# Optimization experiments

Measured on AMD Instinct MI355X. Metric: run time of the kernel, lower is better.

Reference implementation:

```python
import jax, jax.numpy as jnp
import numpy as np
import math

HEAD = 4
B, N, C = 8, 1024, 256


def setup_inputs() -> dict:
    key = jax.random.key(0)
    k1, k2, k3, k4, k5 = jax.random.split(key, 5)
    query = jax.random.normal(k1, (B, N, C), dtype=jnp.float32)
    keyt = jax.random.normal(k2, (B, N, C), dtype=jnp.float32)
    value = jax.random.normal(k3, (B, N, C), dtype=jnp.float32)
    mask = jax.random.randint(k4, (B, N, N), 0, 2).astype(bool)
    dis = jax.random.normal(k5, (B, N, N), dtype=jnp.float32)
    return {"query": query, "key": keyt, "value": value, "mask": mask, "dis": dis}


def reference(query, key, value, mask, dis):
    Bq, Nq, Cq = key.shape
    d = Cq // HEAD
    # split heads: [B,N,C] -> [h,B,N,d]
    q = query.reshape(Bq, Nq, HEAD, d).transpose(2, 0, 1, 3)
    k = key.reshape(Bq, Nq, HEAD, d).transpose(2, 0, 1, 3)
    v = value.reshape(Bq, Nq, HEAD, d).transpose(2, 0, 1, 3)
    # scores: [h,B,N,N]; note: dis added BEFORE scaling, as in the torch code
    scores = jnp.einsum('hbnd,hbmd->hbnm', q, k)
    scores = scores + dis[None]            # dis broadcasts over head dim
    scores = scores / math.sqrt(d)
    scores = jnp.where(mask[None], -jnp.inf, scores)
    p_attn = jax.nn.softmax(scores, axis=-1)
    out = jnp.einsum('hbnm,hbmd->hbnd', p_attn, v)  # [h,B,N,d]
    out = out.transpose(1, 2, 0, 3).reshape(Bq, Nq, Cq)
    return out, p_attn
```

## Files before the change

kernel.cpp:

```cpp
#include <hip/hip_runtime.h>
#include <math.h>

#define HEADS 4
#define BATCH 8
#define SEQ   1024
#define CH    256
#define DH    64
#define RB    16
#define NTHR  512
#define SSTR  1032

typedef float  floatx4  __attribute__((ext_vector_type(4)));
typedef short  shortx8  __attribute__((ext_vector_type(8)));

__device__ __forceinline__ unsigned short f2bf(float f) {
    unsigned u = __float_as_uint(f);
    unsigned r = u + 0x7FFFu + ((u >> 16) & 1u);
    return (unsigned short)(r >> 16);
}
__device__ __forceinline__ float bf2f(unsigned short h) {
    return __uint_as_float(((unsigned)h) << 16);
}
__device__ __forceinline__ shortx8 pack8(float4 a, float4 b) {
    shortx8 r;
    r[0] = (short)f2bf(a.x); r[1] = (short)f2bf(a.y);
    r[2] = (short)f2bf(a.z); r[3] = (short)f2bf(a.w);
    r[4] = (short)f2bf(b.x); r[5] = (short)f2bf(b.y);
    r[6] = (short)f2bf(b.z); r[7] = (short)f2bf(b.w);
    return r;
}

__global__ __launch_bounds__(NTHR, 8)
void attn_mfma(const float* __restrict__ q, const float* __restrict__ k,
               const float* __restrict__ v, const void* __restrict__ maskp,
               const float* __restrict__ dis, float* __restrict__ out,
               float* __restrict__ pout)
{
    __shared__ unsigned short Sraw[RB][SSTR];
    __shared__ float Opart[RB][65];
    __shared__ float invs[RB];

    const int t   = threadIdx.x;
    const int bid = blockIdx.x;
    const int nb  = bid & 63;
    const int hb  = bid >> 6;
    const int b   = hb & (BATCH - 1);
    const int h   = hb >> 3;
    const int n0  = nb * RB;

    const int lane = t & 63;
    const int w    = t >> 6;
    const int ln   = lane & 15;
    const int qd   = lane >> 4;

    int fl;
    {
        const unsigned* mw = (const unsigned*)maskp;
        int found = 0;
        #pragma unroll
        for (int j = 0; j < 16; ++j)
            if (mw[lane * 16 + j] & 0xFFFFFF00u) found = 1;
        fl = (__ballot(found != 0) != 0ULL) ? 1 : 0;
    }
    const unsigned char* mask8  = (const unsigned char*)maskp;
    const int*           mask32 = (const int*)maskp;

    const float* qrow = q + ((size_t)(b * SEQ + n0 + ln)) * CH + h * DH;
    shortx8 aq0, aq1;
    {
        float4 a0 = *(const float4*)(qrow + qd * 8);
        float4 a1 = *(const float4*)(qrow + qd * 8 + 4);
        float4 a2 = *(const float4*)(qrow + 32 + qd * 8);
        float4 a3 = *(const float4*)(qrow + 32 + qd * 8 + 4);
        aq0 = pack8(a0, a1);
        aq1 = pack8(a2, a3);
    }

    const float* kbase = k + ((size_t)(b * SEQ)) * CH + h * DH;
    const float* vbase = v + ((size_t)(b * SEQ)) * CH + h * DH;

    #pragma unroll 2
    for (int mc = 0; mc < 8; ++mc) {
        const int mg = mc * 128 + w * 16 + ln;
        const size_t dibase = ((size_t)(b * SEQ + n0 + qd * 4)) * SEQ + mg;
        float dv[4]; int mk[4];
        #pragma unroll
        for (int r = 0; r < 4; ++r) dv[r] = dis[dibase + (size_t)r * SEQ];
        if (fl) {
            #pragma unroll
            for (int r = 0; r < 4; ++r) mk[r] = mask8[dibase + (size_t)r * SEQ];
        } else {
            #pragma unroll
            for (int r = 0; r < 4; ++r) mk[r] = mask32[dibase + (size_t)r * SEQ];
        }
        const float* krow = kbase + (size_t)mg * CH;
        float4 k0 = *(const float4*)(krow + qd * 8);
        float4 k1 = *(const float4*)(krow + qd * 8 + 4);
        float4 k2 = *(const float4*)(krow + 32 + qd * 8);
        float4 k3 = *(const float4*)(krow + 32 + qd * 8 + 4);

        shortx8 b0 = pack8(k0, k1), b1 = pack8(k2, k3);
        floatx4 acc = {0.f, 0.f, 0.f, 0.f};
        acc = __builtin_amdgcn_mfma_f32_16x16x32_bf16(aq0, b0, acc, 0, 0, 0);
        acc = __builtin_amdgcn_mfma_f32_16x16x32_bf16(aq1, b1, acc, 0, 0, 0);
        #pragma unroll
        for (int r = 0; r < 4; ++r) {
            float sc = mk[r] ? -INFINITY : (acc[r] + dv[r]) * 0.125f;
            Sraw[qd * 4 + r][mg] = f2bf(sc);
        }
    }
    __syncthreads();

    {
        const int r = t >> 5, l = t & 31;
        float mx = -INFINITY;
        #pragma unroll
        for (int j = 0; j < 4; ++j) {
            shortx8 sv = *(const shortx8*)&Sraw[r][j * 256 + l * 8];
            #pragma unroll
            for (int e = 0; e < 8; ++e) mx = fmaxf(mx, bf2f((unsigned short)sv[e]));
        }
        #pragma unroll
        for (int off = 16; off; off >>= 1) mx = fmaxf(mx, __shfl_xor(mx, off, 32));
        float sum = 0.f;
        #pragma unroll
        for (int j = 0; j < 4; ++j) {
            shortx8 sv = *(const shortx8*)&Sraw[r][j * 256 + l * 8];
            shortx8 ev;
            #pragma unroll
            for (int e = 0; e < 8; ++e) {
                float x = __expf(bf2f((unsigned short)sv[e]) - mx);
                sum += x;
                ev[e] = (short)f2bf(x);
            }
            *(shortx8*)&Sraw[r][j * 256 + l * 8] = ev;
        }
        #pragma unroll
        for (int off = 16; off; off >>= 1) sum += __shfl_xor(sum, off, 32);
        if (l == 0) invs[r] = 1.0f / sum;
    }
    __syncthreads();

    {
        float* prow = pout + ((size_t)((h * BATCH + b) * SEQ + n0)) * SEQ;
        #pragma unroll
        for (int i = 0; i < RB; ++i) {
            const float inv = invs[i];
            unsigned pk = *(const unsigned*)&Sraw[i][t * 2];
            float2 pv = { bf2f((unsigned short)(pk & 0xFFFFu)) * inv,
                          bf2f((unsigned short)(pk >> 16)) * inv };
            *(float2*)(prow + (size_t)i * SEQ + t * 2) = pv;
        }
    }

    const int hm = w >> 2;
    const int c  = (w & 3) * 16;
    floatx4 acco = {0.f, 0.f, 0.f, 0.f};
    for (int mc = 0; mc < 8; ++mc) {
        #pragma unroll
        for (int s = 0; s < 2; ++s) {
            const int kb = hm * 512 + mc * 64 + s * 32 + qd * 8;
            float vv[8];
            #pragma unroll
            for (int j = 0; j < 8; ++j)
                vv[j] = vbase[(size_t)(kb + j) * CH + c + ln];
            shortx8 af = *(const shortx8*)&Sraw[ln][kb];
            shortx8 bfv;
            #pragma unroll
            for (int j = 0; j < 8; ++j) bfv[j] = (short)f2bf(vv[j]);
            acco = __builtin_amdgcn_mfma_f32_16x16x32_bf16(af, bfv, acco, 0, 0, 0);
        }
    }
    if (hm == 1) {
        #pragma unroll
        for (int r = 0; r < 4; ++r) Opart[qd * 4 + r][c + ln] = acco[r];
    }
    __syncthreads();
    if (hm == 0) {
        #pragma unroll
        for (int r = 0; r < 4; ++r) {
            int row = qd * 4 + r;
            out[((size_t)(b * SEQ + n0 + row)) * CH + h * DH + c + ln]
                = (acco[r] + Opart[row][c + ln]) * invs[row];
        }
    }
}

extern "C" void kernel_launch(void* const* d_in, const int* in_sizes, int n_in,
                              void* d_out, int out_size, void* d_ws, size_t ws_size,
                              hipStream_t stream) {
    const float* q    = (const float*)d_in[0];
    const float* k    = (const float*)d_in[1];
    const float* v    = (const float*)d_in[2];
    const void*  mask = d_in[3];
    const float* dis  = (const float*)d_in[4];
    float* out  = (float*)d_out;
    float* pout = out + (size_t)BATCH * SEQ * CH;
    (void)d_ws; (void)ws_size;

    attn_mfma<<<HEADS * BATCH * (SEQ / RB), NTHR, 0, stream>>>(
        q, k, v, mask, dis, out, pout);
}
```

Baseline: 313.1 us.

## Pre-convert Q/K to bf16 and V to transposed bf16 in a prep kernel

Adds a prep kernel that converts Q and K to bf16 and writes V as a per-head transposed bf16 array in workspace. The attention kernel then loads bf16 operands directly, with contiguous 16-byte V loads instead of eight strided fp32 gathers plus per-element conversion. The point is to cut the redundant K/V fp32 traffic and conversion work that every row block repeats. The cost is an extra launch and a workspace round trip, and it assumes the workspace is large enough.

```diff
diff --git a/kernel.cpp b/kernel.cpp
--- a/kernel.cpp
+++ b/kernel.cpp
@@ -30,9 +30,55 @@
     return r;
 }
 
+__global__ __launch_bounds__(256)
+void prep(const float* __restrict__ q, const float* __restrict__ k,
+          const float* __restrict__ v, unsigned short* __restrict__ qb,
+          unsigned short* __restrict__ kb, unsigned short* __restrict__ vt)
+{
+    const int t = threadIdx.x;
+    const int bid = blockIdx.x;
+    if (bid < 2048) {
+        const float* src = (bid < 1024) ? q : k;
+        unsigned short* dst = (bid < 1024) ? qb : kb;
+        size_t idx = (size_t)(bid & 1023) * 2048 + (size_t)t * 8;
+        float4 a = *(const float4*)(src + idx);
+        float4 b = *(const float4*)(src + idx + 4);
+        *(shortx8*)(dst + idx) = pack8(a, b);
+        return;
+    }
+    __shared__ unsigned short tl[64][68];
+    const int vb = bid - 2048;
+    const int nt = vb & 15, h = (vb >> 4) & 3, b = vb >> 6;
+    const int n0 = nt * 64;
+    const float* vsrc = v + ((size_t)(b * SEQ + n0)) * CH + h * DH;
+    #pragma unroll
+    for (int it = 0; it < 4; ++it) {
+        int fid = it * 256 + t;
+        int n = fid >> 4, cc = (fid & 15) * 4;
+        float4 x = *(const float4*)(vsrc + (size_t)n * CH + cc);
+        tl[n][cc]     = f2bf(x.x);
+        tl[n][cc + 1] = f2bf(x.y);
+        tl[n][cc + 2] = f2bf(x.z);
+        tl[n][cc + 3] = f2bf(x.w);
+    }
+    __syncthreads();
+    unsigned short* vout = vt + ((size_t)((b * HEADS + h) * DH)) * SEQ + n0;
+    #pragma unroll
+    for (int it = 0; it < 2; ++it) {
+        int cid = it * 256 + t;
+        int d = cid >> 3, nc = cid & 7;
+        shortx8 r;
+        #pragma unroll
+        for (int j = 0; j < 8; ++j) r[j] = (short)tl[nc * 8 + j][d];
+        *(shortx8*)(vout + (size_t)d * SEQ + nc * 8) = r;
+    }
+}
+
 __global__ __launch_bounds__(NTHR, 8)
-void attn_mfma(const float* __restrict__ q, const float* __restrict__ k,
-               const float* __restrict__ v, const void* __restrict__ maskp,
+void attn_mfma(const unsigned short* __restrict__ qb,
+               const unsigned short* __restrict__ kbf,
+               const unsigned short* __restrict__ vt,
+               const void* __restrict__ maskp,
                const float* __restrict__ dis, float* __restrict__ out,
                float* __restrict__ pout)
 {
@@ -65,19 +111,12 @@
     const unsigned char* mask8  = (const unsigned char*)maskp;
     const int*           mask32 = (const int*)maskp;
 
-    const float* qrow = q + ((size_t)(b * SEQ + n0 + ln)) * CH + h * DH;
-    shortx8 aq0, aq1;
-    {
-        float4 a0 = *(const float4*)(qrow + qd * 8);
-        float4 a1 = *(const float4*)(qrow + qd * 8 + 4);
-        float4 a2 = *(const float4*)(qrow + 32 + qd * 8);
-        float4 a3 = *(const float4*)(qrow + 32 + qd * 8 + 4);
-        aq0 = pack8(a0, a1);
-        aq1 = pack8(a2, a3);
-    }
-
-    const float* kbase = k + ((size_t)(b * SEQ)) * CH + h * DH;
-    const float* vbase = v + ((size_t)(b * SEQ)) * CH + h * DH;
+    const unsigned short* qrow = qb + ((size_t)(b * SEQ + n0 + ln)) * CH + h * DH;
+    shortx8 aq0 = *(const shortx8*)(qrow + qd * 8);
+    shortx8 aq1 = *(const shortx8*)(qrow + 32 + qd * 8);
+
+    const unsigned short* kbase = kbf + ((size_t)(b * SEQ)) * CH + h * DH;
+    const unsigned short* vbase = vt + ((size_t)((b * HEADS + h) * DH)) * SEQ;
 
     #pragma unroll 2
     for (int mc = 0; mc < 8; ++mc) {
@@ -93,13 +132,9 @@
             #pragma unroll
             for (int r = 0; r < 4; ++r) mk[r] = mask32[dibase + (size_t)r * SEQ];
         }
-        const float* krow = kbase + (size_t)mg * CH;
-        float4 k0 = *(const float4*)(krow + qd * 8);
-        float4 k1 = *(const float4*)(krow + qd * 8 + 4);
-        float4 k2 = *(const float4*)(krow + 32 + qd * 8);
-        float4 k3 = *(const float4*)(krow + 32 + qd * 8 + 4);
-
-        shortx8 b0 = pack8(k0, k1), b1 = pack8(k2, k3);
+        const unsigned short* krow = kbase + (size_t)mg * CH;
+        shortx8 b0 = *(const shortx8*)(krow + qd * 8);
+        shortx8 b1 = *(const shortx8*)(krow + 32 + qd * 8);
         floatx4 acc = {0.f, 0.f, 0.f, 0.f};
         acc = __builtin_amdgcn_mfma_f32_16x16x32_bf16(aq0, b0, acc, 0, 0, 0);
         acc = __builtin_amdgcn_mfma_f32_16x16x32_bf16(aq1, b1, acc, 0, 0, 0);
@@ -156,18 +191,14 @@
     const int hm = w >> 2;
     const int c  = (w & 3) * 16;
     floatx4 acco = {0.f, 0.f, 0.f, 0.f};
+    const unsigned short* vcol = vbase + (size_t)(c + ln) * SEQ;
+    #pragma unroll 2
     for (int mc = 0; mc < 8; ++mc) {
         #pragma unroll
         for (int s = 0; s < 2; ++s) {
-            const int kb = hm * 512 + mc * 64 + s * 32 + qd * 8;
-            float vv[8];
-            #pragma unroll
-            for (int j = 0; j < 8; ++j)
-                vv[j] = vbase[(size_t)(kb + j) * CH + c + ln];
-            shortx8 af = *(const shortx8*)&Sraw[ln][kb];
-            shortx8 bfv;
-            #pragma unroll
-            for (int j = 0; j < 8; ++j) bfv[j] = (short)f2bf(vv[j]);
+            const int kk = hm * 512 + mc * 64 + s * 32 + qd * 8;
+            shortx8 af  = *(const shortx8*)&Sraw[ln][kk];
+            shortx8 bfv = *(const shortx8*)(vcol + kk);
             acco = __builtin_amdgcn_mfma_f32_16x16x32_bf16(af, bfv, acco, 0, 0, 0);
         }
     }
@@ -196,8 +227,13 @@
     const float* dis  = (const float*)d_in[4];
     float* out  = (float*)d_out;
     float* pout = out + (size_t)BATCH * SEQ * CH;
-    (void)d_ws; (void)ws_size;
-
+
+    unsigned short* qb  = (unsigned short*)d_ws;
+    unsigned short* kbw = qb  + (size_t)BATCH * SEQ * CH;
+    unsigned short* vtw = kbw + (size_t)BATCH * SEQ * CH;
+    (void)ws_size;
+
+    prep<<<2560, 256, 0, stream>>>(q, k, v, qb, kbw, vtw);
     attn_mfma<<<HEADS * BATCH * (SEQ / RB), NTHR, 0, stream>>>(
-        q, k, v, mask, dis, out, pout);
-}
+        qb, kbw, vtw, mask, dis, out, pout);
+}
```

Result: faster. 275.5 us (-12.0%).
